# Kernel optimization log

Hardware: AMD Instinct MI355X
Metric: run time of the kernel (lower is better)

## Reference

```python
import jax, jax.numpy as jnp
import numpy as np

NUM_HEADS = 8
HIDDEN_DIM = 256
QUERY_DIM = 256
HEAD_DIM = HIDDEN_DIM // NUM_HEADS
NORM_FACT = float(HIDDEN_DIM / NUM_HEADS) ** (-0.5)


def setup_inputs() -> dict:
    key = jax.random.key(0)
    k1, k2, k3, k4, k5 = jax.random.split(key, 5)
    B, Q, H, W = 16, 100, 64, 64
    q = jax.random.normal(k1, (B, Q, QUERY_DIM), dtype=jnp.float32)
    k = jax.random.normal(k2, (B, QUERY_DIM, H, W), dtype=jnp.float32)
    mask = jax.random.randint(k3, (B, H, W), 0, 2).astype(jnp.bool_)
    # xavier_uniform for [hidden, query] linear weights
    limit = float(np.sqrt(6.0 / (HIDDEN_DIM + QUERY_DIM)))
    Wq = jax.random.uniform(k4, (HIDDEN_DIM, QUERY_DIM), minval=-limit, maxval=limit, dtype=jnp.float32)
    Wk = jax.random.uniform(k5, (HIDDEN_DIM, QUERY_DIM), minval=-limit, maxval=limit, dtype=jnp.float32)
    bq = jnp.zeros((HIDDEN_DIM,), dtype=jnp.float32)
    bk = jnp.zeros((HIDDEN_DIM,), dtype=jnp.float32)
    return {"q": q, "k": k, "Wq": Wq, "bq": bq, "Wk": Wk, "bk": bk, "mask": mask}


def reference(q, k, Wq, bq, Wk, bk, mask):
    B, Q, _ = q.shape
    _, C, H, W = k.shape
    # q projection: [B, Q, hidden]
    qp = jnp.einsum('bqc,hc->bqh', q, Wq) + bq
    # k projection via 1x1 conv == channelwise linear: [B, hidden, H, W]
    kp = jnp.einsum('bchw,oc->bohw', k, Wk) + bk[None, :, None, None]
    # split heads: qh [B,Q,nh,hd], kh [B,nh,hd,H,W]
    qh = qp.reshape(B, Q, NUM_HEADS, HEAD_DIM)
    kh = kp.reshape(B, NUM_HEADS, HEAD_DIM, H, W)
    # scores [B,Q,nh,H,W]
    weights = jnp.einsum('bqnd,bndhw->bqnhw', qh, kh) * NORM_FACT
    # masked fill: mask [B,H,W] -> broadcast over (Q, heads)
    weights = jnp.where(mask[:, None, None, :, :], -jnp.inf, weights)
    # softmax jointly over (heads, H, W), as in torch flatten(2)
    flat = weights.reshape(B, Q, NUM_HEADS * H * W)
    flat = jax.nn.softmax(flat, axis=-1)
    return flat.reshape(B, Q, NUM_HEADS, H, W)
```

## Files before the change

### kernel.cpp

```cpp
#include <hip/hip_runtime.h>
#include <hip/hip_bf16.h>
#include <math.h>

#define BB 16
#define QQ 100
#define NH 8
#define HWN 4096
#define NORM_FACT 0.17677669529663687f
#define QPAD 112
#define NSLOT 2048

typedef short bf16x8_t __attribute__((ext_vector_type(8)));
typedef float f32x4_t  __attribute__((ext_vector_type(4)));

__device__ __forceinline__ unsigned short bf16bits(float f) {
    __hip_bfloat16 h = __float2bfloat16(f);
    return __builtin_bit_cast(unsigned short, h);
}
__device__ __forceinline__ float bf16tof(unsigned short u) {
    union { unsigned int i; float f; } x; x.i = (unsigned int)u << 16; return x.f;
}

__global__ void k_prep(const float* __restrict__ Wq, const float* __restrict__ Wk,
                       float* __restrict__ WqT, unsigned short* __restrict__ Wkbf) {
    int idx = blockIdx.x;
    int h = threadIdx.x;
    if (idx < 256) {
        WqT[idx * 256 + h] = Wq[h * 256 + idx];
    } else {
        int r = idx - 256;
        Wkbf[r * 256 + h] = bf16bits(Wk[r * 256 + h]);
    }
}

__global__ __launch_bounds__(256) void k_qproj(const float* __restrict__ q,
                                               const float* __restrict__ WqT,
                                               const float* __restrict__ bq,
                                               unsigned short* __restrict__ qphi,
                                               unsigned short* __restrict__ qplo) {
    int blk = blockIdx.x;
    int b = blk / 28, q0 = (blk % 28) * 4;
    int h = threadIdx.x;
    size_t obase = ((size_t)b * QPAD + q0) * 256 + h;
    if (q0 >= QQ) {
#pragma unroll
        for (int i = 0; i < 4; ++i) { qphi[obase + i * 256] = 0; qplo[obase + i * 256] = 0; }
        return;
    }
    __shared__ float qsh[4][256];
    int ibase = (b * QQ + q0) * 256;
#pragma unroll
    for (int i = 0; i < 4; ++i) qsh[i][h] = q[ibase + i * 256 + h];
    __syncthreads();
    float bias = bq[h];
    float a0 = bias, a1 = bias, a2 = bias, a3 = bias;
    for (int c = 0; c < 256; ++c) {
        float wv = WqT[c * 256 + h];
        a0 = fmaf(qsh[0][c], wv, a0);
        a1 = fmaf(qsh[1][c], wv, a1);
        a2 = fmaf(qsh[2][c], wv, a2);
        a3 = fmaf(qsh[3][c], wv, a3);
    }
    float a[4] = {a0 * NORM_FACT, a1 * NORM_FACT, a2 * NORM_FACT, a3 * NORM_FACT};
#pragma unroll
    for (int i = 0; i < 4; ++i) {
        unsigned short hi = bf16bits(a[i]);
        qphi[obase + i * 256] = hi;
        qplo[obase + i * 256] = bf16bits(a[i] - bf16tof(hi));
    }
}

__global__ __launch_bounds__(512) void k_kproj3(const float* __restrict__ k,
                                                const unsigned short* __restrict__ Wkbf,
                                                const float* __restrict__ bk,
                                                unsigned short* __restrict__ kpT) {
    int b = blockIdx.y;
    int hwblk = blockIdx.x * 64;
    int t = threadIdx.x;
    int w = t >> 6, lane = t & 63;
    int hwt = w & 3, oh = w >> 2;
    int n15 = lane & 15, kg = lane >> 4;
    int hw_l = hwt * 16 + n15;

    __shared__ float lds_f[64][140];

    f32x4_t acc[8];
#pragma unroll
    for (int m = 0; m < 8; ++m) acc[m] = f32x4_t{0.f, 0.f, 0.f, 0.f};

    const float* kb = k + (size_t)b * 256 * HWN + hwblk;
    const unsigned short* wbase = Wkbf + ((size_t)(oh * 128 + n15)) * 256 + kg * 8;
    int c_l = t >> 4, l16 = t & 15;

#pragma unroll
    for (int chunk = 0; chunk < 2; ++chunk) {
#pragma unroll
        for (int p = 0; p < 4; ++p) {
            int cc = p * 32 + c_l;
            float4 v = *(const float4*)(kb + (size_t)(chunk * 128 + cc) * HWN + l16 * 4);
            lds_f[l16 * 4 + 0][cc] = v.x;
            lds_f[l16 * 4 + 1][cc] = v.y;
            lds_f[l16 * 4 + 2][cc] = v.z;
            lds_f[l16 * 4 + 3][cc] = v.w;
        }
        __syncthreads();
#pragma unroll
        for (int ksl = 0; ksl < 4; ++ksl) {
            f32x4_t f0 = *(const f32x4_t*)&lds_f[hw_l][ksl * 32 + kg * 8];
            f32x4_t f1 = *(const f32x4_t*)&lds_f[hw_l][ksl * 32 + kg * 8 + 4];
            bf16x8_t bfrag;
#pragma unroll
            for (int j = 0; j < 4; ++j) {
                bfrag[j]     = (short)bf16bits(f0[j]);
                bfrag[4 + j] = (short)bf16bits(f1[j]);
            }
            int ks = chunk * 4 + ksl;
#pragma unroll
            for (int m = 0; m < 8; ++m) {
                bf16x8_t afrag = *reinterpret_cast<const bf16x8_t*>(wbase + (size_t)m * 16 * 256 + ks * 32);
                acc[m] = __builtin_amdgcn_mfma_f32_16x16x32_bf16(afrag, bfrag, acc[m], 0, 0, 0);
            }
        }
        __syncthreads();
    }

    unsigned short* tile2 = (unsigned short*)lds_f;
#pragma unroll
    for (int m = 0; m < 8; ++m) {
        ushort4 pk;
        unsigned short* pkp = (unsigned short*)&pk;
#pragma unroll
        for (int r = 0; r < 4; ++r) {
            int o = oh * 128 + m * 16 + kg * 4 + r;
            pkp[r] = bf16bits(acc[m][r] + bk[o]);
        }
        *(ushort4*)&tile2[(size_t)hw_l * 264 + oh * 128 + m * 16 + kg * 4] = pk;
    }
    __syncthreads();
    int l5 = t & 31;
#pragma unroll
    for (int it = 0; it < 4; ++it) {
        int row = it * 16 + (t >> 5);
        uint4 v = *(const uint4*)&tile2[(size_t)row * 264 + l5 * 8];
        *(uint4*)(kpT + ((size_t)b * HWN + hwblk + row) * 256 + l5 * 8) = v;
    }
}

__global__ __launch_bounds__(256) void k_sums(const unsigned short* __restrict__ qphi,
                                              const unsigned short* __restrict__ qplo,
                                              const unsigned short* __restrict__ kpT,
                                              const int* __restrict__ mask,
                                              float* __restrict__ partial) {
    int hwb = blockIdx.x, n = blockIdx.y, b = blockIdx.z;
    int t = threadIdx.x, w = t >> 6, lane = t & 63;
    int n15 = lane & 15, kg = lane >> 4;
    int hw = hwb * 64 + w * 16 + n15;
    float mm = mask[b * HWN + hw] ? 0.0f : 1.0f;
    bf16x8_t bfr = *reinterpret_cast<const bf16x8_t*>(
        kpT + ((size_t)(b * HWN + hw)) * 256 + n * 32 + kg * 8);
    const unsigned short* ahi_b = qphi + ((size_t)(b * QPAD + n15)) * 256 + n * 32 + kg * 8;
    const unsigned short* alo_b = qplo + ((size_t)(b * QPAD + n15)) * 256 + n * 32 + kg * 8;
    int slot = (hwb * 4 + w) * 8 + n;
    float* pbase = partial + (size_t)b * QPAD * NSLOT + slot;
#pragma unroll
    for (int mt = 0; mt < 7; ++mt) {
        bf16x8_t ahi = *reinterpret_cast<const bf16x8_t*>(ahi_b + (size_t)(mt * 16) * 256);
        bf16x8_t alo = *reinterpret_cast<const bf16x8_t*>(alo_b + (size_t)(mt * 16) * 256);
        f32x4_t a2 = {0.f, 0.f, 0.f, 0.f};
        a2 = __builtin_amdgcn_mfma_f32_16x16x32_bf16(ahi, bfr, a2, 0, 0, 0);
        a2 = __builtin_amdgcn_mfma_f32_16x16x32_bf16(alo, bfr, a2, 0, 0, 0);
#pragma unroll
        for (int r = 0; r < 4; ++r) {
            float v = __expf(a2[r]) * mm;
            v += __shfl_xor(v, 1, 64);
            v += __shfl_xor(v, 2, 64);
            v += __shfl_xor(v, 4, 64);
            v += __shfl_xor(v, 8, 64);
            if (n15 == 0)
                pbase[(size_t)(mt * 16 + kg * 4 + r) * NSLOT] = v;
        }
    }
}

__global__ __launch_bounds__(256) void k_invsum(const float* __restrict__ partial,
                                                float* __restrict__ inv) {
    int blk = blockIdx.x;
    int b = blk / QQ, qq = blk % QQ;
    const float* p = partial + ((size_t)b * QPAD + qq) * NSLOT;
    int t = threadIdx.x;
    float v = 0.0f;
#pragma unroll
    for (int j = 0; j < NSLOT / 256; ++j) v += p[t + j * 256];
#pragma unroll
    for (int off = 32; off; off >>= 1) v += __shfl_xor(v, off, 64);
    __shared__ float red[4];
    if ((t & 63) == 0) red[t >> 6] = v;
    __syncthreads();
    if (t == 0) inv[blk] = 1.0f / (red[0] + red[1] + red[2] + red[3]);
}

__global__ __launch_bounds__(256) void k_write(const unsigned short* __restrict__ qphi,
                                               const unsigned short* __restrict__ qplo,
                                               const unsigned short* __restrict__ kpT,
                                               const int* __restrict__ mask,
                                               const float* __restrict__ inv,
                                               float* __restrict__ out) {
    int hws = blockIdx.x, n = blockIdx.y, b = blockIdx.z;
    int t = threadIdx.x, w = t >> 6, lane = t & 63;
    int n15 = lane & 15, kg = lane >> 4;
    int hw0 = hws * 256 + w * 64;
    float mm[4];
#pragma unroll
    for (int ht = 0; ht < 4; ++ht)
        mm[ht] = mask[b * HWN + hw0 + ht * 16 + n15] ? 0.0f : 1.0f;
    bf16x8_t bf[4];
#pragma unroll
    for (int ht = 0; ht < 4; ++ht)
        bf[ht] = *reinterpret_cast<const bf16x8_t*>(
            kpT + ((size_t)(b * HWN + hw0 + ht * 16 + n15)) * 256 + n * 32 + kg * 8);
    const unsigned short* ahi_b = qphi + ((size_t)(b * QPAD + n15)) * 256 + n * 32 + kg * 8;
    const unsigned short* alo_b = qplo + ((size_t)(b * QPAD + n15)) * 256 + n * 32 + kg * 8;
    __shared__ float lt[4][16][68];
#pragma unroll 1
    for (int qt = 0; qt < 7; ++qt) {
        bf16x8_t ahi = *reinterpret_cast<const bf16x8_t*>(ahi_b + (size_t)(qt * 16) * 256);
        bf16x8_t alo = *reinterpret_cast<const bf16x8_t*>(alo_b + (size_t)(qt * 16) * 256);
        float invq[4];
#pragma unroll
        for (int r = 0; r < 4; ++r) {
            int qrow = qt * 16 + kg * 4 + r;
            invq[r] = (qrow < QQ) ? inv[b * QQ + qrow] : 0.0f;
        }
#pragma unroll
        for (int ht = 0; ht < 4; ++ht) {
            f32x4_t acc = {0.f, 0.f, 0.f, 0.f};
            acc = __builtin_amdgcn_mfma_f32_16x16x32_bf16(ahi, bf[ht], acc, 0, 0, 0);
            acc = __builtin_amdgcn_mfma_f32_16x16x32_bf16(alo, bf[ht], acc, 0, 0, 0);
#pragma unroll
            for (int r = 0; r < 4; ++r)
                lt[w][kg * 4 + r][ht * 16 + n15] = __expf(acc[r]) * mm[ht] * invq[r];
        }
#pragma unroll
        for (int j = 0; j < 4; ++j) {
            int rr = j * 4 + kg;
            int qrow = qt * 16 + rr;
            f32x4_t v4 = *(const f32x4_t*)&lt[w][rr][n15 * 4];
            if (qrow < QQ)
                *(f32x4_t*)(out + (((size_t)(b * QQ + qrow)) * NH + n) * HWN + hw0 + n15 * 4) = v4;
        }
    }
}

extern "C" void kernel_launch(void* const* d_in, const int* in_sizes, int n_in,
                              void* d_out, int out_size, void* d_ws, size_t ws_size,
                              hipStream_t stream) {
    const float* q    = (const float*)d_in[0];
    const float* k    = (const float*)d_in[1];
    const float* Wq   = (const float*)d_in[2];
    const float* bq   = (const float*)d_in[3];
    const float* Wk   = (const float*)d_in[4];
    const float* bk   = (const float*)d_in[5];
    const int*   mask = (const int*)d_in[6];
    float* out = (float*)d_out;

    char* base = (char*)d_ws;
    unsigned short* kpT  = (unsigned short*)(base);
    unsigned short* qphi = (unsigned short*)(base + 33554432);
    unsigned short* qplo = (unsigned short*)(base + 34471936);
    float*  WqT     = (float*)(base + 35389440);
    unsigned short* Wkbf = (unsigned short*)(base + 35651584);
    float*  partial = (float*)(base + 35782656);
    float*  inv     = (float*)(base + 50462720);
    if (ws_size < (size_t)50469120) return;

    k_prep  <<<dim3(512), dim3(256), 0, stream>>>(Wq, Wk, WqT, Wkbf);
    k_qproj <<<dim3(448), dim3(256), 0, stream>>>(q, WqT, bq, qphi, qplo);
    k_kproj3<<<dim3(64, 16), dim3(512), 0, stream>>>(k, Wkbf, bk, kpT);
    k_sums  <<<dim3(64, 8, 16), dim3(256), 0, stream>>>(qphi, qplo, kpT, mask, partial);
    k_invsum<<<dim3(1600), dim3(256), 0, stream>>>(partial, inv);
    k_write <<<dim3(16, 8, 16), dim3(256), 0, stream>>>(qphi, qplo, kpT, mask, inv, out);
}
```

Measured before the change: 203.5 us.

## Accumulate head sums in registers and widen softmax output stores with nontemporal writes

k_sums now loops over all 8 heads inside one block and accumulates exp sums in registers, so it writes 256 partial slots per query row instead of 2048. That cuts partial-buffer traffic and the reduction work in k_invsum. k_write now stages a full 16x256 tile in shared memory, so each wave writes full 1 KB contiguous rows with nontemporal stores. The cost is two block-wide barriers per q-tile and a smaller sums grid with fewer blocks.

Result: faster. 193.6 us (-4.8%).

```diff
diff --git a/kernel.cpp b/kernel.cpp
--- a/kernel.cpp
+++ b/kernel.cpp
@@ -8,7 +8,6 @@
 #define HWN 4096
 #define NORM_FACT 0.17677669529663687f
 #define QPAD 112
-#define NSLOT 2048
 
 typedef short bf16x8_t __attribute__((ext_vector_type(8)));
 typedef float f32x4_t  __attribute__((ext_vector_type(4)));
@@ -151,46 +150,53 @@
                                               const unsigned short* __restrict__ kpT,
                                               const int* __restrict__ mask,
                                               float* __restrict__ partial) {
-    int hwb = blockIdx.x, n = blockIdx.y, b = blockIdx.z;
+    int hwb = blockIdx.x, b = blockIdx.y;
     int t = threadIdx.x, w = t >> 6, lane = t & 63;
     int n15 = lane & 15, kg = lane >> 4;
     int hw = hwb * 64 + w * 16 + n15;
     float mm = mask[b * HWN + hw] ? 0.0f : 1.0f;
-    bf16x8_t bfr = *reinterpret_cast<const bf16x8_t*>(
-        kpT + ((size_t)(b * HWN + hw)) * 256 + n * 32 + kg * 8);
-    const unsigned short* ahi_b = qphi + ((size_t)(b * QPAD + n15)) * 256 + n * 32 + kg * 8;
-    const unsigned short* alo_b = qplo + ((size_t)(b * QPAD + n15)) * 256 + n * 32 + kg * 8;
-    int slot = (hwb * 4 + w) * 8 + n;
-    float* pbase = partial + (size_t)b * QPAD * NSLOT + slot;
-#pragma unroll
-    for (int mt = 0; mt < 7; ++mt) {
-        bf16x8_t ahi = *reinterpret_cast<const bf16x8_t*>(ahi_b + (size_t)(mt * 16) * 256);
-        bf16x8_t alo = *reinterpret_cast<const bf16x8_t*>(alo_b + (size_t)(mt * 16) * 256);
-        f32x4_t a2 = {0.f, 0.f, 0.f, 0.f};
-        a2 = __builtin_amdgcn_mfma_f32_16x16x32_bf16(ahi, bfr, a2, 0, 0, 0);
-        a2 = __builtin_amdgcn_mfma_f32_16x16x32_bf16(alo, bfr, a2, 0, 0, 0);
+    const unsigned short* brow  = kpT  + ((size_t)(b * HWN + hw)) * 256 + kg * 8;
+    const unsigned short* ahi_b = qphi + ((size_t)(b * QPAD + n15)) * 256 + kg * 8;
+    const unsigned short* alo_b = qplo + ((size_t)(b * QPAD + n15)) * 256 + kg * 8;
+    float sums[7][4] = {};
+#pragma unroll 1
+    for (int n = 0; n < NH; ++n) {
+        bf16x8_t bfr = *reinterpret_cast<const bf16x8_t*>(brow + n * 32);
+#pragma unroll
+        for (int mt = 0; mt < 7; ++mt) {
+            bf16x8_t ahi = *reinterpret_cast<const bf16x8_t*>(ahi_b + (size_t)(mt * 16) * 256 + n * 32);
+            bf16x8_t alo = *reinterpret_cast<const bf16x8_t*>(alo_b + (size_t)(mt * 16) * 256 + n * 32);
+            f32x4_t a2 = {0.f, 0.f, 0.f, 0.f};
+            a2 = __builtin_amdgcn_mfma_f32_16x16x32_bf16(ahi, bfr, a2, 0, 0, 0);
+            a2 = __builtin_amdgcn_mfma_f32_16x16x32_bf16(alo, bfr, a2, 0, 0, 0);
+#pragma unroll
+            for (int r = 0; r < 4; ++r)
+                sums[mt][r] += __expf(a2[r]) * mm;
+        }
+    }
+#pragma unroll
+    for (int mt = 0; mt < 7; ++mt)
 #pragma unroll
         for (int r = 0; r < 4; ++r) {
-            float v = __expf(a2[r]) * mm;
+            float v = sums[mt][r];
             v += __shfl_xor(v, 1, 64);
             v += __shfl_xor(v, 2, 64);
             v += __shfl_xor(v, 4, 64);
             v += __shfl_xor(v, 8, 64);
-            if (n15 == 0)
-                pbase[(size_t)(mt * 16 + kg * 4 + r) * NSLOT] = v;
-        }
-    }
+            if (n15 == 0) {
+                int qrow = mt * 16 + kg * 4 + r;
+                partial[((size_t)b * QPAD + qrow) * 256 + hwb * 4 + w] = v;
+            }
+        }
 }
 
 __global__ __launch_bounds__(256) void k_invsum(const float* __restrict__ partial,
                                                 float* __restrict__ inv) {
     int blk = blockIdx.x;
     int b = blk / QQ, qq = blk % QQ;
-    const float* p = partial + ((size_t)b * QPAD + qq) * NSLOT;
+    const float* p = partial + ((size_t)b * QPAD + qq) * 256;
     int t = threadIdx.x;
-    float v = 0.0f;
-#pragma unroll
-    for (int j = 0; j < NSLOT / 256; ++j) v += p[t + j * 256];
+    float v = p[t];
 #pragma unroll
     for (int off = 32; off; off >>= 1) v += __shfl_xor(v, off, 64);
     __shared__ float red[4];
@@ -220,7 +226,7 @@
             kpT + ((size_t)(b * HWN + hw0 + ht * 16 + n15)) * 256 + n * 32 + kg * 8);
     const unsigned short* ahi_b = qphi + ((size_t)(b * QPAD + n15)) * 256 + n * 32 + kg * 8;
     const unsigned short* alo_b = qplo + ((size_t)(b * QPAD + n15)) * 256 + n * 32 + kg * 8;
-    __shared__ float lt[4][16][68];
+    __shared__ float lt[16][260];
 #pragma unroll 1
     for (int qt = 0; qt < 7; ++qt) {
         bf16x8_t ahi = *reinterpret_cast<const bf16x8_t*>(ahi_b + (size_t)(qt * 16) * 256);
@@ -238,16 +244,19 @@
             acc = __builtin_amdgcn_mfma_f32_16x16x32_bf16(alo, bf[ht], acc, 0, 0, 0);
 #pragma unroll
             for (int r = 0; r < 4; ++r)
-                lt[w][kg * 4 + r][ht * 16 + n15] = __expf(acc[r]) * mm[ht] * invq[r];
-        }
+                lt[kg * 4 + r][w * 64 + ht * 16 + n15] = __expf(acc[r]) * mm[ht] * invq[r];
+        }
+        __syncthreads();
 #pragma unroll
         for (int j = 0; j < 4; ++j) {
-            int rr = j * 4 + kg;
-            int qrow = qt * 16 + rr;
-            f32x4_t v4 = *(const f32x4_t*)&lt[w][rr][n15 * 4];
+            int row = w * 4 + j;
+            int qrow = qt * 16 + row;
+            f32x4_t v4 = *(const f32x4_t*)&lt[row][lane * 4];
             if (qrow < QQ)
-                *(f32x4_t*)(out + (((size_t)(b * QQ + qrow)) * NH + n) * HWN + hw0 + n15 * 4) = v4;
-        }
+                __builtin_nontemporal_store(v4,
+                    (f32x4_t*)(out + (((size_t)(b * QQ + qrow)) * NH + n) * HWN + hws * 256 + lane * 4));
+        }
+        __syncthreads();
     }
 }
 
@@ -270,13 +279,13 @@
     float*  WqT     = (float*)(base + 35389440);
     unsigned short* Wkbf = (unsigned short*)(base + 35651584);
     float*  partial = (float*)(base + 35782656);
-    float*  inv     = (float*)(base + 50462720);
-    if (ws_size < (size_t)50469120) return;
+    float*  inv     = (float*)(base + 37617664);
+    if (ws_size < (size_t)37624064) return;
 
     k_prep  <<<dim3(512), dim3(256), 0, stream>>>(Wq, Wk, WqT, Wkbf);
     k_qproj <<<dim3(448), dim3(256), 0, stream>>>(q, WqT, bq, qphi, qplo);
     k_kproj3<<<dim3(64, 16), dim3(512), 0, stream>>>(k, Wkbf, bk, kpT);
-    k_sums  <<<dim3(64, 8, 16), dim3(256), 0, stream>>>(qphi, qplo, kpT, mask, partial);
+    k_sums  <<<dim3(64, 16), dim3(256), 0, stream>>>(qphi, qplo, kpT, mask, partial);
     k_invsum<<<dim3(1600), dim3(256), 0, stream>>>(partial, inv);
     k_write <<<dim3(16, 8, 16), dim3(256), 0, stream>>>(qphi, qplo, kpT, mask, inv, out);
 }
```
